# Kernel optimization log

Hardware: AMD Instinct MI355X
Metric: run time of the kernel (lower is better)

The kernel has to match this reference:

```python
import jax, jax.numpy as jnp
import numpy as np

N_NODES = 50000
N_EDGES = 1_600_000
D_IN, D_HID, D_OUT, K = 128, 50, 10, 5


def setup_inputs() -> dict:
    key = jax.random.key(0)
    ks = jax.random.split(key, 6)
    x = jax.random.normal(ks[0], (N_NODES, D_IN), dtype=jnp.float32)
    edge_index = jax.random.randint(ks[1], (2, N_EDGES), 0, N_NODES, dtype=jnp.int64)
    cheb_w = jax.random.normal(ks[2], (K, D_IN, D_HID), dtype=jnp.float32) * 0.05
    cheb_b = jax.random.normal(ks[3], (D_HID,), dtype=jnp.float32) * 0.05
    fc_w = jax.random.normal(ks[4], (D_HID, D_OUT), dtype=jnp.float32) * 0.1
    fc_b = jax.random.normal(ks[5], (D_OUT,), dtype=jnp.float32) * 0.1
    return {"x": x, "edge_index": edge_index, "cheb_w": cheb_w,
            "cheb_b": cheb_b, "fc_w": fc_w, "fc_b": fc_b}


def reference(x, edge_index, cheb_w, cheb_b, fc_w, fc_b):
    # ChebConv (PyG, normalization='sym', lambda_max=2.0):
    # L_hat = 2L/lambda_max - I = -D^{-1/2} A D^{-1/2} (zero diagonal)
    row, col = edge_index[0], edge_index[1]
    n = x.shape[0]
    deg = jax.ops.segment_sum(jnp.ones_like(row, dtype=x.dtype), row, num_segments=n)
    dinv = jnp.where(deg > 0, jax.lax.rsqrt(jnp.maximum(deg, 1.0)), 0.0)
    w = -dinv[row] * dinv[col]  # [E] edge weights of L_hat

    def prop(h):  # L_hat @ h via gather-scale-scatter
        return jax.ops.segment_sum(w[:, None] * h[col], row, num_segments=n)

    tx0 = x
    tx1 = prop(x)
    out = jnp.einsum('ni,io->no', tx0, cheb_w[0]) + jnp.einsum('ni,io->no', tx1, cheb_w[1])
    for k in range(2, K):
        tx2 = 2.0 * prop(tx1) - tx0
        out = out + jnp.einsum('ni,io->no', tx2, cheb_w[k])
        tx0, tx1 = tx1, tx2
    out = out + cheb_b

    h = jax.nn.relu(out)
    logits = h @ fc_w + fc_b
    return jax.nn.log_softmax(logits, axis=1)
```

## Files before the change

kernel.cpp:

```cpp
#include <hip/hip_runtime.h>
#include <hip/hip_fp16.h>

#define N_NODES 50000
#define N_EDGES 1600000
#define D_IN    128
#define D_HID   50
#define D_OUT   10
#define K_CHEB  5

#define P1_BLOCKS 256
#define EPB       (N_EDGES / P1_BLOCKS)
#define NBUCK     64
#define NB_USED   49
#define BCAP      256

#define WH_ELEMS  (K_CHEB * 64 * D_IN)
#define WH_BLOCKS ((WH_ELEMS + 255) / 256)

#define VROW      64
#define VSTRIDE   ((size_t)(N_NODES + 1) * VROW)

typedef _Float16 half8_t __attribute__((ext_vector_type(8)));
typedef float    f32x4_t __attribute__((ext_vector_type(4)));


__global__ __launch_bounds__(256) void pass1_kernel(const int* __restrict__ row,
                                                    const int* __restrict__ col,
                                                    unsigned int* __restrict__ store,
                                                    int* __restrict__ bcnt,
                                                    const float* __restrict__ W,
                                                    __half* __restrict__ Wh,
                                                    __half* __restrict__ G0,
                                                    __half* __restrict__ v,
                                                    __half* __restrict__ b1) {
    int tid = threadIdx.x;
    int blk = blockIdx.x;
    if (blk >= P1_BLOCKS) {
        int wb = blk - P1_BLOCKS;
        if (wb < WH_BLOCKS) {
            int idx = wb * 256 + tid;
            if (idx < WH_ELEMS) {
                int i = idx & 127;
                int n = (idx >> 7) & 63;
                int t = idx >> 13;
                float vv = (n < D_HID) ? W[t * D_IN * D_HID + i * D_HID + n] : 0.f;
                Wh[idx] = __float2half(vv);
            }
        } else {
            if (tid < D_IN) G0[(size_t)N_NODES * D_IN + tid] = __float2half(0.f);
            if (tid < VROW) {
                v[4 * VSTRIDE + (size_t)N_NODES * VROW + tid] = __float2half(0.f);
                b1[(size_t)N_NODES * VROW + tid] = __float2half(0.f);
            }
        }
        return;
    }
    __shared__ int cnt[NBUCK];
    if (tid < NBUCK) cnt[tid] = 0;
    __syncthreads();
    int base = blk * EPB;
    size_t sb = (size_t)blk * (NBUCK * BCAP);
    for (int i = tid; i < EPB; i += 256) {
        int r = row[base + i];
        int c = col[base + i];
        int b = r >> 10;
        int pos = atomicAdd(&cnt[b], 1);
        if (pos >= BCAP) pos = BCAP - 1;
        store[sb + (b << 8) + pos] = ((unsigned int)(r & 1023) << 16) | (unsigned int)c;
    }
    __syncthreads();
    if (tid < NBUCK) bcnt[blk * NBUCK + tid] = cnt[tid];
}

__global__ __launch_bounds__(1024) void pass2_kernel(const unsigned int* __restrict__ store,
                                                     const int* __restrict__ bcnt,
                                                     int* __restrict__ row_start,
                                                     float* __restrict__ dinv,
                                                     float* __restrict__ dinv2,
                                                     float* __restrict__ sdeg,
                                                     int* __restrict__ ewc) {
    __shared__ int hist[1024];
    __shared__ int off[1024];
    __shared__ int fill[1024];
    __shared__ int sb_part[1024];
    __shared__ int pscan[64];
    __shared__ int s_bbase;
    int tid = threadIdx.x;
    int b = blockIdx.x;

    {
        int bt = tid & 63, seg = tid >> 6;
        int sum = 0;
        for (int s = seg * 16; s < seg * 16 + 16; ++s) sum += bcnt[s * NBUCK + bt];
        sb_part[tid] = sum;
    }
    __syncthreads();
    if (tid < 64) {
        int tot = 0;
        #pragma unroll
        for (int seg = 0; seg < 16; ++seg) tot += sb_part[seg * 64 + tid];
        pscan[tid] = tot;
    }
    __syncthreads();
    for (int o = 1; o < 64; o <<= 1) {
        int vv = (tid < 64 && tid >= o) ? pscan[tid - o] : 0;
        __syncthreads();
        if (tid < 64) pscan[tid] += vv;
        __syncthreads();
    }
    if (tid == 0) {
        s_bbase = (b == 0) ? 0 : pscan[b - 1];
        if (b == 0) row_start[N_NODES] = pscan[63];
    }
    hist[tid] = 0;
    __syncthreads();
    int bbase_b = s_bbase;

    int strip = tid >> 2;
    int sub   = tid & 3;
    int sn = bcnt[strip * NBUCK + b];
    size_t sb = (size_t)strip * (NBUCK * BCAP) + (b << 8);
    for (int i = sub; i < sn; i += 4)
        atomicAdd(&hist[store[sb + i] >> 16], 1);
    __syncthreads();
    int d = hist[tid];
    off[tid] = d;
    __syncthreads();
    for (int o = 1; o < 1024; o <<= 1) {
        int vv = (tid >= o) ? off[tid - o] : 0;
        __syncthreads();
        off[tid] += vv;
        __syncthreads();
    }
    int excl = off[tid] - d + bbase_b;
    __syncthreads();
    hist[tid] = excl;
    fill[tid] = 0;
    int r = (b << 10) + tid;
    if (r < N_NODES) {
        row_start[r] = excl;
        float fd = (float)d;
        dinv[r]  = d ? rsqrtf(fd)  : 0.f;
        dinv2[r] = d ? (1.f / fd)  : 0.f;
        sdeg[r]  = d ? sqrtf(fd)   : 0.f;
    }
    __syncthreads();
    for (int i = sub; i < sn; i += 4) {
        unsigned int vv = store[sb + i];
        int rl = vv >> 16;
        int c = vv & 0xffff;
        int p = atomicAdd(&fill[rl], 1);
        ewc[hist[rl] + p] = c;
    }
}

__global__ void g0_kernel(const float* __restrict__ x, const float* __restrict__ dinv,
                          __half* __restrict__ g0) {
    int i = blockIdx.x * blockDim.x + threadIdx.x;
    if (i < N_NODES * (D_IN / 4)) {
        int row = i >> 5;
        float d = dinv[row];
        float4 f = ((const float4*)x)[i];
        __half2 a = __float22half2_rn(make_float2(f.x * d, f.y * d));
        __half2 b = __float22half2_rn(make_float2(f.z * d, f.w * d));
        uint2 u;
        u.x = *(unsigned int*)&a;
        u.y = *(unsigned int*)&b;
        ((uint2*)g0)[i] = u;
    }
}

__global__ __launch_bounds__(256) void vgemm_kernel(const __half* __restrict__ g0,
                                                    const __half* __restrict__ Wh,
                                                    __half* __restrict__ v) {
    __shared__ __half ts[64 * 72];
    int tid = threadIdx.x;
    int lane = tid & 63;
    int wv = __builtin_amdgcn_readfirstlane(tid >> 6);
    int row0 = blockIdx.x * 64;
    int m = lane & 15;
    int quad = lane >> 4;

    int arow = row0 + wv * 16 + m;
    if (arow > N_NODES) arow = N_NODES;

    half8_t a[4];
    #pragma unroll
    for (int s = 0; s < 4; ++s)
        a[s] = *(const half8_t*)(g0 + (size_t)arow * D_IN + s * 32 + quad * 8);

    for (int t = 0; t < K_CHEB; ++t) {
        f32x4_t acc[4];
        #pragma unroll
        for (int j = 0; j < 4; ++j) acc[j] = (f32x4_t)0.f;
        const __half* Wt = Wh + t * (64 * D_IN);
        #pragma unroll
        for (int s = 0; s < 4; ++s) {
            int ko = s * 32 + quad * 8;
            #pragma unroll
            for (int j = 0; j < 4; ++j) {
                half8_t b = *(const half8_t*)(Wt + (j * 16 + m) * D_IN + ko);
                acc[j] = __builtin_amdgcn_mfma_f32_16x16x32_f16(a[s], b, acc[j], 0, 0, 0);
            }
        }
        #pragma unroll
        for (int j = 0; j < 4; ++j) {
            int c = j * 16 + m;
            #pragma unroll
            for (int rr = 0; rr < 4; ++rr) {
                int lrow = wv * 16 + quad * 4 + rr;
                ts[lrow * 72 + c] = __float2half(acc[j][rr]);
            }
        }
        __syncthreads();
        {
            int lrow = tid >> 2, part = tid & 3;
            int grow = row0 + lrow;
            if (grow < N_NODES) {
                const uint4* s16 = (const uint4*)(ts + lrow * 72 + part * 16);
                uint4 q0 = s16[0], q1 = s16[1];
                uint4* dst = (uint4*)(v + t * VSTRIDE + (size_t)grow * VROW + part * 16);
                dst[0] = q0;
                dst[1] = q1;
            }
        }
        __syncthreads();
    }
}

__global__ __launch_bounds__(512) void prop_kernel(const int* __restrict__ row_start,
                                                   const int* __restrict__ ewc,
                                                   const float* __restrict__ dinv2,
                                                   const __half* __restrict__ src,
                                                   const __half* __restrict__ addv,
                                                   const __half* __restrict__ subv,
                                                   float alphaM, int do_sub,
                                                   __half* __restrict__ dst) {
    int tid = threadIdx.x;
    int lane = tid & 63;
    int wv = __builtin_amdgcn_readfirstlane(tid >> 6);
    int r = blockIdx.x * 8 + wv;
    int e0 = row_start[r], e1 = row_start[r + 1];
    float fac = -alphaM * dinv2[r];
    int l = lane & 31;
    int g = lane >> 5;
    const __half2* src2 = (const __half2*)src;
    float ax = 0.f, ay = 0.f;
    for (int e = e0; e < e1; e += 16) {
        #pragma unroll
        for (int i = 0; i < 8; ++i) {
            int ca = ewc[e + 2 * i];
            int cb = ewc[e + 2 * i + 1];
            int c = g ? cb : ca;
            if (e + 2 * i + g >= e1) c = N_NODES;
            float2 f = __half22float2(src2[(size_t)c * (VROW / 2) + l]);
            ax += f.x;
            ay += f.y;
        }
    }
    ax += __shfl_xor(ax, 32);
    ay += __shfl_xor(ay, 32);
    if (g == 0) {
        size_t o = (size_t)r * (VROW / 2) + l;
        float2 av = __half22float2(((const __half2*)addv)[o]);
        float r0 = av.x + fac * ax;
        float r1 = av.y + fac * ay;
        if (do_sub) {
            float2 sv = __half22float2(((const __half2*)subv)[o]);
            r0 -= sv.x;
            r1 -= sv.y;
        }
        ((__half2*)dst)[o] = __float22half2_rn(make_float2(r0, r1));
    }
}

__global__ __launch_bounds__(256) void final_kernel(const __half* __restrict__ S,
                                                    const float* __restrict__ sdeg,
                                                    const float* __restrict__ cheb_b,
                                                    const float* __restrict__ fc_w,
                                                    const float* __restrict__ fc_b,
                                                    float* __restrict__ out) {
    int r = blockIdx.x * blockDim.x + threadIdx.x;
    if (r >= N_NODES) return;
    float sc = sdeg[r];
    const __half2* s2 = (const __half2*)(S + (size_t)r * VROW);
    float h[D_HID];
    #pragma unroll
    for (int i = 0; i < D_HID / 2; ++i) {
        float2 f = __half22float2(s2[i]);
        float v0 = sc * f.x + cheb_b[2 * i];
        float v1 = sc * f.y + cheb_b[2 * i + 1];
        h[2 * i]     = v0 > 0.f ? v0 : 0.f;
        h[2 * i + 1] = v1 > 0.f ? v1 : 0.f;
    }
    float lg[D_OUT];
    #pragma unroll
    for (int o = 0; o < D_OUT; ++o) lg[o] = fc_b[o];
    #pragma unroll 2
    for (int i = 0; i < D_HID; ++i) {
        float hv = h[i];
        #pragma unroll
        for (int o = 0; o < D_OUT; ++o) lg[o] += hv * fc_w[i * D_OUT + o];
    }
    float mx = lg[0];
    #pragma unroll
    for (int o = 1; o < D_OUT; ++o) mx = fmaxf(mx, lg[o]);
    float s = 0.f;
    #pragma unroll
    for (int o = 0; o < D_OUT; ++o) s += __expf(lg[o] - mx);
    float ls = __logf(s);
    size_t oo = (size_t)r * D_OUT;
    #pragma unroll
    for (int o = 0; o < D_OUT; ++o) out[oo + o] = lg[o] - mx - ls;
}

extern "C" void kernel_launch(void* const* d_in, const int* in_sizes, int n_in,
                              void* d_out, int out_size, void* d_ws, size_t ws_size,
                              hipStream_t stream) {
    const float* x      = (const float*)d_in[0];
    const int*   edge   = (const int*)d_in[1];
    const float* cheb_w = (const float*)d_in[2];
    const float* cheb_b = (const float*)d_in[3];
    const float* fc_w   = (const float*)d_in[4];
    const float* fc_b   = (const float*)d_in[5];
    float* out = (float*)d_out;

    const int* erow = edge;
    const int* ecol = edge + N_EDGES;

    uintptr_t p = ((uintptr_t)d_ws + 255) & ~(uintptr_t)255;
    auto alloc = [&](size_t bytes) {
        uintptr_t q = p;
        p = (p + bytes + 255) & ~(uintptr_t)255;
        return (void*)q;
    };
    unsigned int* store = (unsigned int*)alloc((size_t)P1_BLOCKS * NBUCK * BCAP * 4);
    int*    bcnt      = (int*)alloc((size_t)P1_BLOCKS * NBUCK * 4);
    int*    row_start = (int*)alloc((size_t)(N_NODES + 1) * 4);
    float*  dinv      = (float*)alloc((size_t)N_NODES * 4);
    float*  dinv2     = (float*)alloc((size_t)N_NODES * 4);
    float*  sdeg      = (float*)alloc((size_t)N_NODES * 4);
    int*    ewc       = (int*)alloc((size_t)(N_EDGES + 32) * 4);
    __half* Wh        = (__half*)alloc((size_t)WH_ELEMS * 2);
    __half* g0        = (__half*)alloc((size_t)(N_NODES + 1) * D_IN * 2);
    __half* v         = (__half*)alloc(5 * VSTRIDE * 2);
    __half* b1        = (__half*)alloc(VSTRIDE * 2);

    __half* b3 = (__half*)store;
    __half* b2 = (__half*)store + VSTRIDE;
    __half* S  = g0;

    pass1_kernel<<<P1_BLOCKS + WH_BLOCKS + 1, 256, 0, stream>>>(
        erow, ecol, store, bcnt, cheb_w, Wh, g0, v, b1);
    pass2_kernel<<<NB_USED, 1024, 0, stream>>>(store, bcnt, row_start,
                                               dinv, dinv2, sdeg, ewc);
    hipMemsetAsync(b3 + (size_t)N_NODES * VROW, 0, VROW * 2, stream);
    hipMemsetAsync(b2 + (size_t)N_NODES * VROW, 0, VROW * 2, stream);

    const int C4 = (N_NODES * D_IN / 4 + 255) / 256;
    g0_kernel<<<C4, 256, 0, stream>>>(x, dinv, g0);

    const int GBK = (N_NODES + 63) / 64;
    vgemm_kernel<<<GBK, 256, 0, stream>>>(g0, Wh, v);

    __half* v0 = v;
    __half* v1 = v + 1 * VSTRIDE;
    __half* v2 = v + 2 * VSTRIDE;
    __half* v3 = v + 3 * VSTRIDE;
    __half* v4 = v + 4 * VSTRIDE;
    const int PB = N_NODES / 8;
    prop_kernel<<<PB, 512, 0, stream>>>(row_start, ewc, dinv2, v4, v3, v3, 2.f, 0, b3);
    prop_kernel<<<PB, 512, 0, stream>>>(row_start, ewc, dinv2, b3, v2, v4, 2.f, 1, b2);
    prop_kernel<<<PB, 512, 0, stream>>>(row_start, ewc, dinv2, b2, v1, b3, 2.f, 1, b1);
    prop_kernel<<<PB, 512, 0, stream>>>(row_start, ewc, dinv2, b1, v0, b2, 1.f, 1, S);

    final_kernel<<<(N_NODES + 255) / 256, 256, 0, stream>>>(S, sdeg, cheb_b,
                                                            fc_w, fc_b, out);
}
```

Measured before the change: 316.7 us.

## Fuse x scaling into MFMA GEMM and widen prop gathers to 8-byte loads

Removes the separate g0 kernel. The GEMM now reads fp32 x directly, converts it to half in registers, and applies the dinv row scaling after the MFMA. The GEMM swaps operand roles so each lane holds a node's outputs and stores them directly, dropping the LDS staging and barriers. The propagation kernel now has 16 lanes per edge, each loading 8 bytes, so four edges are gathered per wavefront iteration. The cost is extra shuffle reductions, and the GEMM now writes scattered 8-byte stores.

```diff
diff --git a/kernel.cpp b/kernel.cpp
--- a/kernel.cpp
+++ b/kernel.cpp
@@ -30,7 +30,6 @@
                                                     int* __restrict__ bcnt,
                                                     const float* __restrict__ W,
                                                     __half* __restrict__ Wh,
-                                                    __half* __restrict__ G0,
                                                     __half* __restrict__ v,
                                                     __half* __restrict__ b1) {
     int tid = threadIdx.x;
@@ -47,7 +46,6 @@
                 Wh[idx] = __float2half(vv);
             }
         } else {
-            if (tid < D_IN) G0[(size_t)N_NODES * D_IN + tid] = __float2half(0.f);
             if (tid < VROW) {
                 v[4 * VSTRIDE + (size_t)N_NODES * VROW + tid] = __float2half(0.f);
                 b1[(size_t)N_NODES * VROW + tid] = __float2half(0.f);
@@ -154,77 +152,60 @@
     }
 }
 
-__global__ void g0_kernel(const float* __restrict__ x, const float* __restrict__ dinv,
-                          __half* __restrict__ g0) {
-    int i = blockIdx.x * blockDim.x + threadIdx.x;
-    if (i < N_NODES * (D_IN / 4)) {
-        int row = i >> 5;
-        float d = dinv[row];
-        float4 f = ((const float4*)x)[i];
-        __half2 a = __float22half2_rn(make_float2(f.x * d, f.y * d));
-        __half2 b = __float22half2_rn(make_float2(f.z * d, f.w * d));
-        uint2 u;
-        u.x = *(unsigned int*)&a;
-        u.y = *(unsigned int*)&b;
-        ((uint2*)g0)[i] = u;
-    }
-}
-
-__global__ __launch_bounds__(256) void vgemm_kernel(const __half* __restrict__ g0,
+__global__ __launch_bounds__(512) void vgemm_kernel(const float* __restrict__ x,
+                                                    const float* __restrict__ dinv,
                                                     const __half* __restrict__ Wh,
                                                     __half* __restrict__ v) {
-    __shared__ __half ts[64 * 72];
     int tid = threadIdx.x;
     int lane = tid & 63;
     int wv = __builtin_amdgcn_readfirstlane(tid >> 6);
-    int row0 = blockIdx.x * 64;
     int m = lane & 15;
     int quad = lane >> 4;
 
-    int arow = row0 + wv * 16 + m;
-    if (arow > N_NODES) arow = N_NODES;
-
-    half8_t a[4];
-    #pragma unroll
-    for (int s = 0; s < 4; ++s)
-        a[s] = *(const half8_t*)(g0 + (size_t)arow * D_IN + s * 32 + quad * 8);
+    int node = (blockIdx.x * 8 + wv) * 16 + m;
+    bool ok = (node < N_NODES);
+    int ln = ok ? node : (N_NODES - 1);
+    float dv = ok ? dinv[node] : 0.f;
+
+    half8_t bfr[4];
+    #pragma unroll
+    for (int ks = 0; ks < 4; ++ks) {
+        const float4* xr = (const float4*)(x + (size_t)ln * D_IN + ks * 32 + quad * 8);
+        float4 fA = xr[0], fB = xr[1];
+        half8_t h;
+        h[0] = (_Float16)fA.x; h[1] = (_Float16)fA.y;
+        h[2] = (_Float16)fA.z; h[3] = (_Float16)fA.w;
+        h[4] = (_Float16)fB.x; h[5] = (_Float16)fB.y;
+        h[6] = (_Float16)fB.z; h[7] = (_Float16)fB.w;
+        bfr[ks] = h;
+    }
 
     for (int t = 0; t < K_CHEB; ++t) {
+        const __half* Wt = Wh + t * (64 * D_IN);
         f32x4_t acc[4];
         #pragma unroll
-        for (int j = 0; j < 4; ++j) acc[j] = (f32x4_t)0.f;
-        const __half* Wt = Wh + t * (64 * D_IN);
-        #pragma unroll
-        for (int s = 0; s < 4; ++s) {
-            int ko = s * 32 + quad * 8;
+        for (int jt = 0; jt < 4; ++jt) acc[jt] = (f32x4_t)0.f;
+        #pragma unroll
+        for (int ks = 0; ks < 4; ++ks) {
+            int ko = ks * 32 + quad * 8;
             #pragma unroll
-            for (int j = 0; j < 4; ++j) {
-                half8_t b = *(const half8_t*)(Wt + (j * 16 + m) * D_IN + ko);
-                acc[j] = __builtin_amdgcn_mfma_f32_16x16x32_f16(a[s], b, acc[j], 0, 0, 0);
+            for (int jt = 0; jt < 4; ++jt) {
+                half8_t a = *(const half8_t*)(Wt + (jt * 16 + m) * D_IN + ko);
+                acc[jt] = __builtin_amdgcn_mfma_f32_16x16x32_f16(a, bfr[ks], acc[jt], 0, 0, 0);
             }
         }
-        #pragma unroll
-        for (int j = 0; j < 4; ++j) {
-            int c = j * 16 + m;
+        if (ok) {
+            __half* dst = v + t * VSTRIDE + (size_t)node * VROW + quad * 4;
             #pragma unroll
-            for (int rr = 0; rr < 4; ++rr) {
-                int lrow = wv * 16 + quad * 4 + rr;
-                ts[lrow * 72 + c] = __float2half(acc[j][rr]);
+            for (int jt = 0; jt < 4; ++jt) {
+                __half2 h0 = __float22half2_rn(make_float2(acc[jt][0] * dv, acc[jt][1] * dv));
+                __half2 h1 = __float22half2_rn(make_float2(acc[jt][2] * dv, acc[jt][3] * dv));
+                uint2 u;
+                u.x = *(unsigned int*)&h0;
+                u.y = *(unsigned int*)&h1;
+                *(uint2*)(dst + jt * 16) = u;
             }
         }
-        __syncthreads();
-        {
-            int lrow = tid >> 2, part = tid & 3;
-            int grow = row0 + lrow;
-            if (grow < N_NODES) {
-                const uint4* s16 = (const uint4*)(ts + lrow * 72 + part * 16);
-                uint4 q0 = s16[0], q1 = s16[1];
-                uint4* dst = (uint4*)(v + t * VSTRIDE + (size_t)grow * VROW + part * 16);
-                dst[0] = q0;
-                dst[1] = q1;
-            }
-        }
-        __syncthreads();
     }
 }
 
@@ -242,35 +223,51 @@
     int r = blockIdx.x * 8 + wv;
     int e0 = row_start[r], e1 = row_start[r + 1];
     float fac = -alphaM * dinv2[r];
-    int l = lane & 31;
-    int g = lane >> 5;
-    const __half2* src2 = (const __half2*)src;
-    float ax = 0.f, ay = 0.f;
-    for (int e = e0; e < e1; e += 16) {
+    int l = lane & 15;
+    int g = lane >> 4;
+    const uint2* src8 = (const uint2*)src;
+    float a0 = 0.f, a1 = 0.f, a2 = 0.f, a3 = 0.f;
+    for (int e = e0; e < e1; e += 32) {
         #pragma unroll
         for (int i = 0; i < 8; ++i) {
-            int ca = ewc[e + 2 * i];
-            int cb = ewc[e + 2 * i + 1];
-            int c = g ? cb : ca;
-            if (e + 2 * i + g >= e1) c = N_NODES;
-            float2 f = __half22float2(src2[(size_t)c * (VROW / 2) + l]);
-            ax += f.x;
-            ay += f.y;
-        }
-    }
-    ax += __shfl_xor(ax, 32);
-    ay += __shfl_xor(ay, 32);
+            int base = e + 4 * i;
+            int c0 = ewc[base + 0];
+            int c1 = ewc[base + 1];
+            int c2 = ewc[base + 2];
+            int c3 = ewc[base + 3];
+            int cl = (g & 2) ? ((g & 1) ? c3 : c2) : ((g & 1) ? c1 : c0);
+            if (base + g >= e1) cl = N_NODES;
+            uint2 u = src8[(size_t)cl * 16 + l];
+            float2 f0 = __half22float2(*(__half2*)&u.x);
+            float2 f1 = __half22float2(*(__half2*)&u.y);
+            a0 += f0.x; a1 += f0.y; a2 += f1.x; a3 += f1.y;
+        }
+    }
+    a0 += __shfl_xor(a0, 16); a1 += __shfl_xor(a1, 16);
+    a2 += __shfl_xor(a2, 16); a3 += __shfl_xor(a3, 16);
+    a0 += __shfl_xor(a0, 32); a1 += __shfl_xor(a1, 32);
+    a2 += __shfl_xor(a2, 32); a3 += __shfl_xor(a3, 32);
     if (g == 0) {
-        size_t o = (size_t)r * (VROW / 2) + l;
-        float2 av = __half22float2(((const __half2*)addv)[o]);
-        float r0 = av.x + fac * ax;
-        float r1 = av.y + fac * ay;
+        size_t o = (size_t)r * 16 + l;
+        uint2 av = ((const uint2*)addv)[o];
+        float2 av0 = __half22float2(*(__half2*)&av.x);
+        float2 av1 = __half22float2(*(__half2*)&av.y);
+        float r0 = av0.x + fac * a0;
+        float r1 = av0.y + fac * a1;
+        float r2 = av1.x + fac * a2;
+        float r3 = av1.y + fac * a3;
         if (do_sub) {
-            float2 sv = __half22float2(((const __half2*)subv)[o]);
-            r0 -= sv.x;
-            r1 -= sv.y;
-        }
-        ((__half2*)dst)[o] = __float22half2_rn(make_float2(r0, r1));
+            uint2 sv = ((const uint2*)subv)[o];
+            float2 sv0 = __half22float2(*(__half2*)&sv.x);
+            float2 sv1 = __half22float2(*(__half2*)&sv.y);
+            r0 -= sv0.x; r1 -= sv0.y; r2 -= sv1.x; r3 -= sv1.y;
+        }
+        __half2 h0 = __float22half2_rn(make_float2(r0, r1));
+        __half2 h1 = __float22half2_rn(make_float2(r2, r3));
+        uint2 u;
+        u.x = *(unsigned int*)&h0;
+        u.y = *(unsigned int*)&h1;
+        ((uint2*)dst)[o] = u;
     }
 }
 
@@ -342,26 +339,23 @@
     float*  sdeg      = (float*)alloc((size_t)N_NODES * 4);
     int*    ewc       = (int*)alloc((size_t)(N_EDGES + 32) * 4);
     __half* Wh        = (__half*)alloc((size_t)WH_ELEMS * 2);
-    __half* g0        = (__half*)alloc((size_t)(N_NODES + 1) * D_IN * 2);
+    __half* Sbuf      = (__half*)alloc(VSTRIDE * 2);
     __half* v         = (__half*)alloc(5 * VSTRIDE * 2);
     __half* b1        = (__half*)alloc(VSTRIDE * 2);
 
     __half* b3 = (__half*)store;
     __half* b2 = (__half*)store + VSTRIDE;
-    __half* S  = g0;
+    __half* S  = Sbuf;
 
     pass1_kernel<<<P1_BLOCKS + WH_BLOCKS + 1, 256, 0, stream>>>(
-        erow, ecol, store, bcnt, cheb_w, Wh, g0, v, b1);
+        erow, ecol, store, bcnt, cheb_w, Wh, v, b1);
     pass2_kernel<<<NB_USED, 1024, 0, stream>>>(store, bcnt, row_start,
                                                dinv, dinv2, sdeg, ewc);
     hipMemsetAsync(b3 + (size_t)N_NODES * VROW, 0, VROW * 2, stream);
     hipMemsetAsync(b2 + (size_t)N_NODES * VROW, 0, VROW * 2, stream);
 
-    const int C4 = (N_NODES * D_IN / 4 + 255) / 256;
-    g0_kernel<<<C4, 256, 0, stream>>>(x, dinv, g0);
-
-    const int GBK = (N_NODES + 63) / 64;
-    vgemm_kernel<<<GBK, 256, 0, stream>>>(g0, Wh, v);
+    const int GBK = (N_NODES + 127) / 128;
+    vgemm_kernel<<<GBK, 512, 0, stream>>>(x, dinv, Wh, v);
 
     __half* v0 = v;
     __half* v1 = v + 1 * VSTRIDE;
```

Measured after the change: 331.2 us. +4.6%, slower.
